# Kernel tuning notes

Hardware: AMD Instinct MI355X
Metric: run time of the kernel (lower is better)

Reference implementation:

```python
import jax, jax.numpy as jnp
import numpy as np

N = 50000          # number of points
C = 64             # num_clusters (embedding width)
K_RAD = 32         # radius graph max_num_neighbors
K_KNN = 10         # knn graph k


def setup_inputs() -> dict:
    key = jax.random.key(0)
    ks = jax.random.split(key, 8)
    x0 = jax.random.normal(ks[0], (N, 3), jnp.float32)
    pos0 = jax.random.normal(ks[1], (N, 3), jnp.float32)
    # R0/t0 come from rigid_fitting in the original (external helper); use
    # orthonormal matrices from batched QR as realistic per-point rotations.
    A = jax.random.normal(ks[2], (N, 3, 3), jnp.float32)
    R0, _ = jnp.linalg.qr(A)
    t0 = jax.random.normal(ks[3], (N, 3), jnp.float32) * 0.1
    # pool1 k=1 assignment: point i -> cluster assign01[i]
    assign01 = jax.random.randint(ks[4], (N,), 0, C, dtype=jnp.int32)
    # radius graph edges (source, target): each point has K_RAD neighbors
    radius_src = jax.random.randint(ks[5], (N * K_RAD,), 0, N, dtype=jnp.int32)
    radius_dst = jnp.repeat(jnp.arange(N, dtype=jnp.int32), K_RAD)
    # knn-10 graph edges used by WeightedAvg
    knn_src = jax.random.randint(ks[6], (N * K_KNN,), 0, N, dtype=jnp.int32)
    knn_dst = jnp.repeat(jnp.arange(N, dtype=jnp.int32), K_KNN)
    return dict(x0=x0, pos0=pos0, R0=R0, t0=t0, assign01=assign01,
                radius_src=radius_src, radius_dst=radius_dst,
                knn_src=knn_src, knn_dst=knn_dst)


def _rigid_layer(xfeat, pos0, x0, R0, t0, src, dst):
    # RigidPropModule.message + max aggregation (nn=None, lin1: w=-1, b=0.01)
    Ri = R0[dst]                     # [E,3,3] target-side rotation
    ti = t0[dst]                     # [E,3]
    posj = pos0[src]                 # [E,3]
    xj = x0[src]                     # [E,3]
    pred = jnp.einsum('eij,ej->ei', Ri, posj) + ti
    d = jnp.sum((pred - xj) ** 2, axis=-1, keepdims=True)   # [E,1]
    w = jax.nn.sigmoid(-d + 0.01)
    msg = w * xfeat[src]             # [E,C]
    agg = jax.ops.segment_max(msg, dst, num_segments=xfeat.shape[0])
    # messages are non-negative; nodes with no edges get 0 (torch_scatter fill)
    return jnp.maximum(agg, 0.0)


def reference(x0, pos0, R0, t0, assign01, radius_src, radius_dst, knn_src, knn_dst):
    n = x0.shape[0]
    # scatter_add of one-hot cluster embeddings back to points
    emb = jnp.zeros((n, C), jnp.float32).at[jnp.arange(n), assign01].add(1.0)
    m1 = _rigid_layer(emb, pos0, x0, R0, t0, radius_src, radius_dst)
    m2 = _rigid_layer(m1, pos0, x0, R0, t0, radius_src, radius_dst)
    m3 = _rigid_layer(m2, pos0, x0, R0, t0, radius_src, radius_dst)
    m4 = _rigid_layer(m2, pos0, x0, R0, t0, radius_src, radius_dst)
    m5 = _rigid_layer(m2, pos0, x0, R0, t0, radius_src, radius_dst)
    msg = jnp.stack([m1.sum(-1), m2.sum(-1), m3.sum(-1),
                     m4.sum(-1), m5.sum(-1)], axis=-1)      # [N,5]
    # predictor: Linear(5,1) with w=ones, b=-17, then sigmoid
    conf = jax.nn.sigmoid(msg.sum(-1, keepdims=True) - 17.0)  # [N,1]
    # WeightedAvg over knn edges: out[t] = sum_s conf[s]*val[s] / sum_s conf[s]
    cw = conf[knn_src]                                       # [E,1]
    num_R = jax.ops.segment_sum(cw * R0.reshape(n, 9)[knn_src], knn_dst, num_segments=n)
    num_t = jax.ops.segment_sum(cw * t0[knn_src], knn_dst, num_segments=n)
    den = jax.ops.segment_sum(cw, knn_dst, num_segments=n) + 1e-8
    R_out = (num_R / den).reshape(n, 3, 3)
    t_out = num_t / den
    x_out = jnp.einsum('nij,nj->ni', R_out, pos0) + t_out
    return x_out, R_out, t_out
```

## Files before the change

### kernel.cpp

```cpp
#include <hip/hip_runtime.h>
#include <hip/hip_fp16.h>
#include <math.h>

#define N_PTS 50000
#define C_DIM 64
#define K_RAD 32
#define K_KNN 10
#define E_RAD (N_PTS * K_RAD)

__device__ inline __half2 hmax2(__half2 a, __half2 b) {
    __half2 d;
    asm("v_pk_max_f16 %0, %1, %2" : "=v"(d) : "v"(a), "v"(b));
    return d;
}

__device__ inline __half2 shfl_xor_h2(__half2 v, int mask) {
    int i = *(int*)&v;
    int r = __shfl_xor(i, mask);
    return *(__half2*)&r;
}

__global__ void pack_tables_kernel(const float* __restrict__ pos0,
                                   const float* __restrict__ x0,
                                   const int* __restrict__ assign,
                                   const float* __restrict__ R0,
                                   const float* __restrict__ t0,
                                   float4* __restrict__ geo,
                                   float4* __restrict__ rt4) {
    int i = blockIdx.x * blockDim.x + threadIdx.x;
    if (i >= N_PTS) return;
    geo[i * 2 + 0] = make_float4(pos0[3 * i], pos0[3 * i + 1], pos0[3 * i + 2], x0[3 * i]);
    geo[i * 2 + 1] = make_float4(x0[3 * i + 1], x0[3 * i + 2], __int_as_float(assign[i]), 0.0f);
    const float* R = R0 + 9 * i;
    rt4[i * 4 + 0] = make_float4(R[0], R[1], R[2], R[3]);
    rt4[i * 4 + 1] = make_float4(R[4], R[5], R[6], R[7]);
    rt4[i * 4 + 2] = make_float4(R[8], t0[3 * i], t0[3 * i + 1], t0[3 * i + 2]);
}

__global__ void ew_layer1_kernel(const float4* __restrict__ geo,
                                 const float* __restrict__ R0,
                                 const float* __restrict__ t0,
                                 const int* __restrict__ src,
                                 unsigned int* __restrict__ packed,
                                 __half* __restrict__ m1,
                                 float* __restrict__ sum1) {
    __shared__ int lm[4][C_DIM];
    int wave = (blockIdx.x * blockDim.x + threadIdx.x) >> 6;
    int lane = threadIdx.x & 63;
    int wslot = threadIdx.x >> 6;
    lm[wslot][lane] = 0;
    int nb = __builtin_amdgcn_readfirstlane(wave);
    int e = lane >> 1;
    int part = lane & 1;
    int s = src[nb * K_RAD + e];
    float4 g = geo[s * 2 + part];
    float ox = __shfl_xor(g.x, 1);
    float oy = __shfl_xor(g.y, 1);
    float oz = __shfl_xor(g.z, 1);
    __syncthreads();
    if (part == 0) {
        const float* R = R0 + nb * 9;
        const float* T = t0 + nb * 3;
        float r0 = R[0] * g.x + R[1] * g.y + R[2] * g.z + T[0] - g.w;
        float r1 = R[3] * g.x + R[4] * g.y + R[5] * g.z + T[1] - ox;
        float r2 = R[6] * g.x + R[7] * g.y + R[8] * g.z + T[2] - oy;
        float dsq = r0 * r0 + r1 * r1 + r2 * r2;
        float w = 1.0f / (1.0f + __expf(dsq - 0.01f));
        unsigned int wb = (unsigned int)__half_as_ushort(__float2half_rn(w));
        packed[nb * K_RAD + e] = ((unsigned int)s << 16) | wb;
        atomicMax(&lm[wslot][__float_as_int(oz)], __float_as_int(w));
    }
    __syncthreads();
    float m = __int_as_float(lm[wslot][lane]);
    if (lane < 32) {
        float lo = __int_as_float(lm[wslot][2 * lane]);
        float hi = __int_as_float(lm[wslot][2 * lane + 1]);
        *(__half2*)(m1 + wave * C_DIM + 2 * lane) = __floats2half2_rn(lo, hi);
    }
    float ssum = m;
#pragma unroll
    for (int off = 32; off > 0; off >>= 1) ssum += __shfl_down(ssum, off);
    if (lane == 0) sum1[wave] = ssum;
}

__global__ void layer_pk_kernel(const unsigned int* __restrict__ packed,
                                const __half* __restrict__ xin,
                                __half* __restrict__ xout,
                                float* __restrict__ sum_out) {
    int wave = (blockIdx.x * blockDim.x + threadIdx.x) >> 6;
    int lane = threadIdx.x & 63;
    if (wave >= N_PTS) return;
    int eslot = lane >> 3;
    int cpos = lane & 7;
    uint4 pv = ((const uint4*)(packed + wave * K_RAD))[eslot];
    unsigned int pes[4] = {pv.x, pv.y, pv.z, pv.w};
    __half2 a0 = __float2half2_rn(0.0f), a1 = a0, a2 = a0, a3 = a0;
#pragma unroll
    for (int p = 0; p < 4; ++p) {
        unsigned int pe = pes[p];
        float4 f = *(const float4*)(xin + (pe >> 16) * C_DIM + cpos * 8);
        __half2* h = (__half2*)&f;
        __half2 w2 = __half2half2(__ushort_as_half((unsigned short)(pe & 0xffffu)));
        a0 = hmax2(a0, __hmul2(w2, h[0]));
        a1 = hmax2(a1, __hmul2(w2, h[1]));
        a2 = hmax2(a2, __hmul2(w2, h[2]));
        a3 = hmax2(a3, __hmul2(w2, h[3]));
    }
#pragma unroll
    for (int off = 8; off < 64; off <<= 1) {
        a0 = hmax2(a0, shfl_xor_h2(a0, off));
        a1 = hmax2(a1, shfl_xor_h2(a1, off));
        a2 = hmax2(a2, shfl_xor_h2(a2, off));
        a3 = hmax2(a3, shfl_xor_h2(a3, off));
    }
    if (eslot == 0) {
        float4 o;
        __half2* oh = (__half2*)&o;
        oh[0] = a0; oh[1] = a1; oh[2] = a2; oh[3] = a3;
        ((float4*)(xout + wave * C_DIM))[cpos] = o;
    }
    float2 v0 = __half22float2(a0), v1 = __half22float2(a1);
    float2 v2 = __half22float2(a2), v3 = __half22float2(a3);
    float s = v0.x + v0.y + v1.x + v1.y + v2.x + v2.y + v3.x + v3.y;
#pragma unroll
    for (int off = 1; off < 8; off <<= 1) s += __shfl_xor(s, off);
    if (lane == 0) sum_out[wave] = s;
}

__global__ void layer3_conf_pk_kernel(const unsigned int* __restrict__ packed,
                                      const __half* __restrict__ xin,
                                      const float* __restrict__ sum1,
                                      const float* __restrict__ sum2,
                                      float* __restrict__ rt4f) {
    int wave = (blockIdx.x * blockDim.x + threadIdx.x) >> 6;
    int lane = threadIdx.x & 63;
    if (wave >= N_PTS) return;
    int eslot = lane >> 3;
    int cpos = lane & 7;
    uint4 pv = ((const uint4*)(packed + wave * K_RAD))[eslot];
    unsigned int pes[4] = {pv.x, pv.y, pv.z, pv.w};
    __half2 a0 = __float2half2_rn(0.0f), a1 = a0, a2 = a0, a3 = a0;
#pragma unroll
    for (int p = 0; p < 4; ++p) {
        unsigned int pe = pes[p];
        float4 f = *(const float4*)(xin + (pe >> 16) * C_DIM + cpos * 8);
        __half2* h = (__half2*)&f;
        __half2 w2 = __half2half2(__ushort_as_half((unsigned short)(pe & 0xffffu)));
        a0 = hmax2(a0, __hmul2(w2, h[0]));
        a1 = hmax2(a1, __hmul2(w2, h[1]));
        a2 = hmax2(a2, __hmul2(w2, h[2]));
        a3 = hmax2(a3, __hmul2(w2, h[3]));
    }
#pragma unroll
    for (int off = 8; off < 64; off <<= 1) {
        a0 = hmax2(a0, shfl_xor_h2(a0, off));
        a1 = hmax2(a1, shfl_xor_h2(a1, off));
        a2 = hmax2(a2, shfl_xor_h2(a2, off));
        a3 = hmax2(a3, shfl_xor_h2(a3, off));
    }
    float2 v0 = __half22float2(a0), v1 = __half22float2(a1);
    float2 v2 = __half22float2(a2), v3 = __half22float2(a3);
    float s = v0.x + v0.y + v1.x + v1.y + v2.x + v2.y + v3.x + v3.y;
#pragma unroll
    for (int off = 1; off < 8; off <<= 1) s += __shfl_xor(s, off);
    if (lane == 0) {
        float tot = sum1[wave] + sum2[wave] + 3.0f * s - 17.0f;
        rt4f[wave * 16 + 12] = 1.0f / (1.0f + __expf(-tot));
    }
}

__global__ void wavg_kernel(const int* __restrict__ knn_src,
                            const float4* __restrict__ rt4,
                            const float* __restrict__ pos0,
                            float* __restrict__ out) {
    int gid = blockIdx.x * blockDim.x + threadIdx.x;
    int lane = gid & 63;
    int t = (gid >> 6) * 16 + (lane >> 2);
    int part = lane & 3;
    if (t >= N_PTS) return;
    float4 acc = make_float4(0.f, 0.f, 0.f, 0.f);
    for (int j = 0; j < K_KNN; ++j) {
        int s = knn_src[t * K_KNN + j];
        float4 q = rt4[s * 4 + part];
        float c = __shfl(q.x, lane | 3);
        if (part == 3) {
            acc.x += c;
        } else {
            acc.x += c * q.x; acc.y += c * q.y;
            acc.z += c * q.z; acc.w += c * q.w;
        }
    }
    float den = __shfl(acc.x, lane | 3) + 1e-8f;
    float inv = 1.0f / den;
    float4 sc = make_float4(acc.x * inv, acc.y * inv, acc.z * inv, acc.w * inv);
    int base = lane & ~3;
    float R3 = __shfl(sc.w, base + 0);
    float R6 = __shfl(sc.z, base + 1);
    float R7 = __shfl(sc.w, base + 1);
    float t0v = __shfl(sc.y, base + 2);
    float t1v = __shfl(sc.z, base + 2);
    float px = pos0[t * 3 + 0], py = pos0[t * 3 + 1], pz = pos0[t * 3 + 2];
    float* Rout = out + N_PTS * 3;
    float* tout = out + N_PTS * 12;
    if (part == 0) {
        out[t * 3 + 0] = sc.x * px + sc.y * py + sc.z * pz + t0v;
        Rout[t * 9 + 0] = sc.x; Rout[t * 9 + 1] = sc.y;
        Rout[t * 9 + 2] = sc.z; Rout[t * 9 + 3] = sc.w;
    } else if (part == 1) {
        out[t * 3 + 1] = R3 * px + sc.x * py + sc.y * pz + t1v;
        Rout[t * 9 + 4] = sc.x; Rout[t * 9 + 5] = sc.y;
        Rout[t * 9 + 6] = sc.z; Rout[t * 9 + 7] = sc.w;
    } else if (part == 2) {
        out[t * 3 + 2] = R6 * px + R7 * py + sc.x * pz + sc.w;
        Rout[t * 9 + 8] = sc.x;
        tout[t * 3 + 0] = sc.y; tout[t * 3 + 1] = sc.z; tout[t * 3 + 2] = sc.w;
    }
}

extern "C" void kernel_launch(void* const* d_in, const int* in_sizes, int n_in,
                              void* d_out, int out_size, void* d_ws, size_t ws_size,
                              hipStream_t stream) {
    const float* x0 = (const float*)d_in[0];
    const float* pos0 = (const float*)d_in[1];
    const float* R0 = (const float*)d_in[2];
    const float* t0 = (const float*)d_in[3];
    const int* assign01 = (const int*)d_in[4];
    const int* radius_src = (const int*)d_in[5];
    const int* knn_src = (const int*)d_in[7];

    char* ws = (char*)d_ws;
    unsigned int* packed = (unsigned int*)ws;
    __half* mA = (__half*)(ws + 6400000);
    __half* mB = (__half*)(ws + 12800000);
    float4* geo = (float4*)(ws + 19200000);
    float4* rt4 = (float4*)(ws + 20800000);
    float* sum1 = (float*)(ws + 24000000);
    float* sum2 = (float*)(ws + 24200000);
    float* out = (float*)d_out;

    int layer_blocks = (N_PTS * 64 + 255) / 256;

    pack_tables_kernel<<<(N_PTS + 255) / 256, 256, 0, stream>>>(
        pos0, x0, assign01, R0, t0, geo, rt4);

    ew_layer1_kernel<<<layer_blocks, 256, 0, stream>>>(
        geo, R0, t0, radius_src, packed, mA, sum1);

    layer_pk_kernel<<<layer_blocks, 256, 0, stream>>>(
        packed, mA, mB, sum2);

    layer3_conf_pk_kernel<<<layer_blocks, 256, 0, stream>>>(
        packed, mB, sum1, sum2, (float*)rt4);

    wavg_kernel<<<(N_PTS * 4 + 255) / 256, 256, 0, stream>>>(
        knn_src, rt4, pos0, out);
}
```

Measured before the change: 141.0 us.

## Pack more nodes per block in edge-weight and max-aggregation kernels

```diff
diff --git a/kernel.cpp b/kernel.cpp
--- a/kernel.cpp
+++ b/kernel.cpp
@@ -44,59 +44,78 @@
                                  unsigned int* __restrict__ packed,
                                  __half* __restrict__ m1,
                                  float* __restrict__ sum1) {
-    __shared__ int lm[4][C_DIM];
-    int wave = (blockIdx.x * blockDim.x + threadIdx.x) >> 6;
-    int lane = threadIdx.x & 63;
-    int wslot = threadIdx.x >> 6;
-    lm[wslot][lane] = 0;
-    int nb = __builtin_amdgcn_readfirstlane(wave);
-    int e = lane >> 1;
-    int part = lane & 1;
-    int s = src[nb * K_RAD + e];
-    float4 g = geo[s * 2 + part];
-    float ox = __shfl_xor(g.x, 1);
-    float oy = __shfl_xor(g.y, 1);
-    float oz = __shfl_xor(g.z, 1);
+    __shared__ int lm[16][C_DIM];
+    __shared__ float ldsR[16 * 9];
+    __shared__ float ldsT[16 * 3];
+    int tid = threadIdx.x;
+    int blk = blockIdx.x;
+    ((int*)lm)[tid] = 0;
+    ((int*)lm)[tid + 256] = 0;
+    ((int*)lm)[tid + 512] = 0;
+    ((int*)lm)[tid + 768] = 0;
+    if (tid < 144) ldsR[tid] = R0[blk * 144 + tid];
+    if (tid < 48) ldsT[tid] = t0[blk * 48 + tid];
+    int nl = tid >> 4;
+    int ng = blk * 16 + nl;
+    int e0 = tid & 15, e1 = e0 + 16;
+    int s0 = src[ng * K_RAD + e0];
+    int s1 = src[ng * K_RAD + e1];
+    float4 g0a = geo[s0 * 2 + 0];
+    float4 g0b = geo[s0 * 2 + 1];
+    float4 g1a = geo[s1 * 2 + 0];
+    float4 g1b = geo[s1 * 2 + 1];
     __syncthreads();
-    if (part == 0) {
-        const float* R = R0 + nb * 9;
-        const float* T = t0 + nb * 3;
-        float r0 = R[0] * g.x + R[1] * g.y + R[2] * g.z + T[0] - g.w;
-        float r1 = R[3] * g.x + R[4] * g.y + R[5] * g.z + T[1] - ox;
-        float r2 = R[6] * g.x + R[7] * g.y + R[8] * g.z + T[2] - oy;
-        float dsq = r0 * r0 + r1 * r1 + r2 * r2;
-        float w = 1.0f / (1.0f + __expf(dsq - 0.01f));
-        unsigned int wb = (unsigned int)__half_as_ushort(__float2half_rn(w));
-        packed[nb * K_RAD + e] = ((unsigned int)s << 16) | wb;
-        atomicMax(&lm[wslot][__float_as_int(oz)], __float_as_int(w));
-    }
+    const float* R = ldsR + nl * 9;
+    const float* T = ldsT + nl * 3;
+    float r0 = R[0] * g0a.x + R[1] * g0a.y + R[2] * g0a.z + T[0] - g0a.w;
+    float r1 = R[3] * g0a.x + R[4] * g0a.y + R[5] * g0a.z + T[1] - g0b.x;
+    float r2 = R[6] * g0a.x + R[7] * g0a.y + R[8] * g0a.z + T[2] - g0b.y;
+    float d0 = r0 * r0 + r1 * r1 + r2 * r2;
+    float w0 = 1.0f / (1.0f + __expf(d0 - 0.01f));
+    float u0 = R[0] * g1a.x + R[1] * g1a.y + R[2] * g1a.z + T[0] - g1a.w;
+    float u1 = R[3] * g1a.x + R[4] * g1a.y + R[5] * g1a.z + T[1] - g1b.x;
+    float u2 = R[6] * g1a.x + R[7] * g1a.y + R[8] * g1a.z + T[2] - g1b.y;
+    float d1 = u0 * u0 + u1 * u1 + u2 * u2;
+    float w1 = 1.0f / (1.0f + __expf(d1 - 0.01f));
+    packed[ng * K_RAD + e0] =
+        ((unsigned int)s0 << 16) | (unsigned int)__half_as_ushort(__float2half_rn(w0));
+    packed[ng * K_RAD + e1] =
+        ((unsigned int)s1 << 16) | (unsigned int)__half_as_ushort(__float2half_rn(w1));
+    atomicMax(&lm[nl][__float_as_int(g0b.z)], __float_as_int(w0));
+    atomicMax(&lm[nl][__float_as_int(g1b.z)], __float_as_int(w1));
     __syncthreads();
-    float m = __int_as_float(lm[wslot][lane]);
-    if (lane < 32) {
-        float lo = __int_as_float(lm[wslot][2 * lane]);
-        float hi = __int_as_float(lm[wslot][2 * lane + 1]);
-        *(__half2*)(m1 + wave * C_DIM + 2 * lane) = __floats2half2_rn(lo, hi);
-    }
-    float ssum = m;
-#pragma unroll
-    for (int off = 32; off > 0; off >>= 1) ssum += __shfl_down(ssum, off);
-    if (lane == 0) sum1[wave] = ssum;
+    int c0 = (tid & 15) * 4;
+    float v0 = __int_as_float(lm[nl][c0 + 0]);
+    float v1 = __int_as_float(lm[nl][c0 + 1]);
+    float v2 = __int_as_float(lm[nl][c0 + 2]);
+    float v3 = __int_as_float(lm[nl][c0 + 3]);
+    __half2 h01 = __floats2half2_rn(v0, v1);
+    __half2 h23 = __floats2half2_rn(v2, v3);
+    uint2 uo = make_uint2(*(unsigned int*)&h01, *(unsigned int*)&h23);
+    *(uint2*)(m1 + ng * C_DIM + c0) = uo;
+    float s = v0 + v1 + v2 + v3;
+    s += __shfl_down(s, 8);
+    s += __shfl_down(s, 4);
+    s += __shfl_down(s, 2);
+    s += __shfl_down(s, 1);
+    if ((tid & 15) == 0) sum1[ng] = s;
 }
 
 __global__ void layer_pk_kernel(const unsigned int* __restrict__ packed,
                                 const __half* __restrict__ xin,
                                 __half* __restrict__ xout,
                                 float* __restrict__ sum_out) {
-    int wave = (blockIdx.x * blockDim.x + threadIdx.x) >> 6;
-    int lane = threadIdx.x & 63;
-    if (wave >= N_PTS) return;
-    int eslot = lane >> 3;
+    int gid = blockIdx.x * blockDim.x + threadIdx.x;
+    int lane = gid & 63;
+    int node = (gid >> 6) * 2 + (lane >> 5);
+    int eslot = (lane >> 3) & 3;
     int cpos = lane & 7;
-    uint4 pv = ((const uint4*)(packed + wave * K_RAD))[eslot];
-    unsigned int pes[4] = {pv.x, pv.y, pv.z, pv.w};
+    const uint4* pk4 = (const uint4*)(packed + node * K_RAD + eslot * 8);
+    uint4 q0 = pk4[0], q1 = pk4[1];
+    unsigned int pes[8] = {q0.x, q0.y, q0.z, q0.w, q1.x, q1.y, q1.z, q1.w};
     __half2 a0 = __float2half2_rn(0.0f), a1 = a0, a2 = a0, a3 = a0;
 #pragma unroll
-    for (int p = 0; p < 4; ++p) {
+    for (int p = 0; p < 8; ++p) {
         unsigned int pe = pes[p];
         float4 f = *(const float4*)(xin + (pe >> 16) * C_DIM + cpos * 8);
         __half2* h = (__half2*)&f;
@@ -107,7 +126,7 @@
         a3 = hmax2(a3, __hmul2(w2, h[3]));
     }
 #pragma unroll
-    for (int off = 8; off < 64; off <<= 1) {
+    for (int off = 8; off <= 16; off <<= 1) {
         a0 = hmax2(a0, shfl_xor_h2(a0, off));
         a1 = hmax2(a1, shfl_xor_h2(a1, off));
         a2 = hmax2(a2, shfl_xor_h2(a2, off));
@@ -117,14 +136,15 @@
         float4 o;
         __half2* oh = (__half2*)&o;
         oh[0] = a0; oh[1] = a1; oh[2] = a2; oh[3] = a3;
-        ((float4*)(xout + wave * C_DIM))[cpos] = o;
+        ((float4*)(xout + node * C_DIM))[cpos] = o;
     }
     float2 v0 = __half22float2(a0), v1 = __half22float2(a1);
     float2 v2 = __half22float2(a2), v3 = __half22float2(a3);
     float s = v0.x + v0.y + v1.x + v1.y + v2.x + v2.y + v3.x + v3.y;
-#pragma unroll
-    for (int off = 1; off < 8; off <<= 1) s += __shfl_xor(s, off);
-    if (lane == 0) sum_out[wave] = s;
+    s += __shfl_xor(s, 1);
+    s += __shfl_xor(s, 2);
+    s += __shfl_xor(s, 4);
+    if ((lane & 31) == 0) sum_out[node] = s;
 }
 
 __global__ void layer3_conf_pk_kernel(const unsigned int* __restrict__ packed,
@@ -132,16 +152,17 @@
                                       const float* __restrict__ sum1,
                                       const float* __restrict__ sum2,
                                       float* __restrict__ rt4f) {
-    int wave = (blockIdx.x * blockDim.x + threadIdx.x) >> 6;
-    int lane = threadIdx.x & 63;
-    if (wave >= N_PTS) return;
-    int eslot = lane >> 3;
+    int gid = blockIdx.x * blockDim.x + threadIdx.x;
+    int lane = gid & 63;
+    int node = (gid >> 6) * 2 + (lane >> 5);
+    int eslot = (lane >> 3) & 3;
     int cpos = lane & 7;
-    uint4 pv = ((const uint4*)(packed + wave * K_RAD))[eslot];
-    unsigned int pes[4] = {pv.x, pv.y, pv.z, pv.w};
+    const uint4* pk4 = (const uint4*)(packed + node * K_RAD + eslot * 8);
+    uint4 q0 = pk4[0], q1 = pk4[1];
+    unsigned int pes[8] = {q0.x, q0.y, q0.z, q0.w, q1.x, q1.y, q1.z, q1.w};
     __half2 a0 = __float2half2_rn(0.0f), a1 = a0, a2 = a0, a3 = a0;
 #pragma unroll
-    for (int p = 0; p < 4; ++p) {
+    for (int p = 0; p < 8; ++p) {
         unsigned int pe = pes[p];
         float4 f = *(const float4*)(xin + (pe >> 16) * C_DIM + cpos * 8);
         __half2* h = (__half2*)&f;
@@ -152,7 +173,7 @@
         a3 = hmax2(a3, __hmul2(w2, h[3]));
     }
 #pragma unroll
-    for (int off = 8; off < 64; off <<= 1) {
+    for (int off = 8; off <= 16; off <<= 1) {
         a0 = hmax2(a0, shfl_xor_h2(a0, off));
         a1 = hmax2(a1, shfl_xor_h2(a1, off));
         a2 = hmax2(a2, shfl_xor_h2(a2, off));
@@ -161,11 +182,12 @@
     float2 v0 = __half22float2(a0), v1 = __half22float2(a1);
     float2 v2 = __half22float2(a2), v3 = __half22float2(a3);
     float s = v0.x + v0.y + v1.x + v1.y + v2.x + v2.y + v3.x + v3.y;
-#pragma unroll
-    for (int off = 1; off < 8; off <<= 1) s += __shfl_xor(s, off);
-    if (lane == 0) {
-        float tot = sum1[wave] + sum2[wave] + 3.0f * s - 17.0f;
-        rt4f[wave * 16 + 12] = 1.0f / (1.0f + __expf(-tot));
+    s += __shfl_xor(s, 1);
+    s += __shfl_xor(s, 2);
+    s += __shfl_xor(s, 4);
+    if ((lane & 31) == 0) {
+        float tot = sum1[node] + sum2[node] + 3.0f * s - 17.0f;
+        rt4f[node * 16 + 12] = 1.0f / (1.0f + __expf(-tot));
     }
 }
 
@@ -238,18 +260,16 @@
     float* sum2 = (float*)(ws + 24200000);
     float* out = (float*)d_out;
 
-    int layer_blocks = (N_PTS * 64 + 255) / 256;
-
     pack_tables_kernel<<<(N_PTS + 255) / 256, 256, 0, stream>>>(
         pos0, x0, assign01, R0, t0, geo, rt4);
 
-    ew_layer1_kernel<<<layer_blocks, 256, 0, stream>>>(
+    ew_layer1_kernel<<<N_PTS / 16, 256, 0, stream>>>(
         geo, R0, t0, radius_src, packed, mA, sum1);
 
-    layer_pk_kernel<<<layer_blocks, 256, 0, stream>>>(
+    layer_pk_kernel<<<N_PTS / 8, 256, 0, stream>>>(
         packed, mA, mB, sum2);
 
-    layer3_conf_pk_kernel<<<layer_blocks, 256, 0, stream>>>(
+    layer3_conf_pk_kernel<<<N_PTS / 8, 256, 0, stream>>>(
         packed, mB, sum1, sum2, (float*)rt4);
 
     wavg_kernel<<<(N_PTS * 4 + 255) / 256, 256, 0, stream>>>(
```

Measured after the change: 139.0 us. Within noise of the previous version (-1.4%).
